# Kernel tuning notes

Hardware: AMD Instinct MI355X
Metric: run time of the kernel (lower is better)

The kernel has to match this reference:

```python
import jax, jax.numpy as jnp
from jax import lax
import numpy as np

T, B, I = 512, 64, 1024
L, H = 2, 1024

def setup_inputs() -> dict:
    key = jax.random.key(0)
    k1, k2, k3 = jax.random.split(key, 3)
    scale = 1.0 / np.sqrt(H)
    return {
        "x": jax.random.normal(k1, (T, B, I), dtype=jnp.float32),
        "w_ih": jax.random.normal(k2, (L, 4 * H, I), dtype=jnp.float32) * scale,
        "w_hh": jax.random.normal(k3, (L, 4 * H, H), dtype=jnp.float32) * scale,
        "b_ih": jnp.zeros((L, 4 * H), dtype=jnp.float32),
        "b_hh": jnp.zeros((L, 4 * H), dtype=jnp.float32),
    }

def _lstm_layer(seq, wi, wh, b):
    # seq: [T, B, D]; wi: [4H, D]; wh: [4H, H]; b: [4H]
    Bsz = seq.shape[1]
    Hh = wh.shape[1]
    # precompute input projection for all timesteps (one big GEMM)
    xin = jnp.einsum('tbd,gd->tbg', seq, wi) + b  # [T, B, 4H]
    def step(carry, xt):
        h, c = carry
        gates = xt + h @ wh.T  # [B, 4H]
        i, f, g, o = jnp.split(gates, 4, axis=1)
        c = jax.nn.sigmoid(f) * c + jax.nn.sigmoid(i) * jnp.tanh(g)
        h = jax.nn.sigmoid(o) * jnp.tanh(c)
        return (h, c), h
    h0 = jnp.zeros((Bsz, Hh), seq.dtype)
    c0 = jnp.zeros((Bsz, Hh), seq.dtype)
    (hn, cn), out = lax.scan(step, (h0, c0), xin)
    return out, hn, cn

def reference(x, w_ih, w_hh, b_ih, b_hh):
    seq = x
    h_n, c_n = [], []
    for l in range(w_hh.shape[0]):
        seq, hn, cn = _lstm_layer(seq, w_ih[l], w_hh[l], b_ih[l] + b_hh[l])
        h_n.append(hn)
        c_n.append(cn)
    return seq, jnp.stack(h_n, 0), jnp.stack(c_n, 0)
```

## Files before the change

### kernel.cpp

```cpp
#include <hip/hip_runtime.h>
#include <cstddef>
#include <cstdint>

#define T_LEN   512
#define BATCH   64
#define IN_DIM  1024
#define HID     1024
#define GATES   4096
#define NLAYERS 2
#define BH      (BATCH * HID)
#define LBLK    256
#define NBLK    512

typedef __bf16 bf16;
typedef __bf16 bf16x8 __attribute__((ext_vector_type(8)));
typedef float  f32x4  __attribute__((ext_vector_type(4)));

__global__ __launch_bounds__(256) void cvt_bf16(const float* __restrict__ in,
                                                bf16* __restrict__ out, int n4) {
    int i = blockIdx.x * blockDim.x + threadIdx.x;
    if (i >= n4) return;
    float4 v = ((const float4*)in)[i];
    bf16 o[4] = {(bf16)v.x, (bf16)v.y, (bf16)v.z, (bf16)v.w};
    *(uint2*)(out + 4 * (size_t)i) = *(uint2*)o;
}

#define GEMV8(XP, BB)                                                          \
    _Pragma("unroll")                                                          \
    for (int q = 0; q < 8; ++q) {                                              \
        const int k0 = q * 32;                                                 \
        acc0 = __builtin_amdgcn_mfma_f32_16x16x32_bf16(                        \
            *(const bf16x8*)((XP) + k0),       *(const bf16x8*)((BB) + k0),       acc0, 0, 0, 0); \
        acc1 = __builtin_amdgcn_mfma_f32_16x16x32_bf16(                        \
            *(const bf16x8*)((XP) + 256 + k0), *(const bf16x8*)((BB) + 256 + k0), acc1, 0, 0, 0); \
        acc2 = __builtin_amdgcn_mfma_f32_16x16x32_bf16(                        \
            *(const bf16x8*)((XP) + 512 + k0), *(const bf16x8*)((BB) + 512 + k0), acc2, 0, 0, 0); \
        acc3 = __builtin_amdgcn_mfma_f32_16x16x32_bf16(                        \
            *(const bf16x8*)((XP) + 768 + k0), *(const bf16x8*)((BB) + 768 + k0), acc3, 0, 0, 0); \
    }

__global__ __launch_bounds__(256) void lstm_pipe(
    const bf16*  __restrict__ wi0,
    const bf16*  __restrict__ wh0,
    const bf16*  __restrict__ wi1,
    const bf16*  __restrict__ wh1,
    const float* __restrict__ bih,
    const float* __restrict__ bhh,
    const bf16*  __restrict__ xbf,
    bf16*        __restrict__ h0seq,
    bf16*        __restrict__ h1seq,
    float*       __restrict__ outf,
    float*       __restrict__ hf0,
    float*       __restrict__ hf1,
    float*       __restrict__ cb0,
    float*       __restrict__ cb1,
    unsigned*    __restrict__ bar)
{
    __shared__ bf16  Bi[16 * 1032];
    __shared__ bf16  Bh[16 * 1032];
    __shared__ float sg[4 * 272];

    const int bk   = blockIdx.x;
    const bool isL1 = (bk >= LBLK);
    const int lk   = bk & (LBLK - 1);
    const int j0   = lk * 4;
    const int tid  = threadIdx.x;
    const int lane = tid & 63;
    const int wv   = tid >> 6;
    const int m0   = wv * 16;
    const int quad = lane >> 4;
    const int l16  = lane & 15;

    unsigned* flags   = bar;
    unsigned* release = bar + 768;

    const bf16* wiL = isL1 ? wi1 : wi0;
    const bf16* whL = isL1 ? wh1 : wh0;
    const int   boff = isL1 ? GATES : 0;
    bf16*       hW  = isL1 ? h1seq : h0seq;
    float*      hfL = isL1 ? hf1 : hf0;
    float*      cbL = isL1 ? cb1 : cb0;

    #pragma unroll
    for (int i = 0; i < 8; ++i) {
        int flat = i * 256 + tid;
        int row  = flat >> 7;
        int k16  = flat & 127;
        int grr  = (row >> 2) * 1024 + j0 + (row & 3);
        *(uint4*)&Bi[row * 1032 + k16 * 8] =
            *(const uint4*)(wiL + (size_t)grr * IN_DIM + k16 * 8);
        *(uint4*)&Bh[row * 1032 + k16 * 8] =
            *(const uint4*)(whL + (size_t)grr * HID + k16 * 8);
    }

    const int cb = m0 + l16;
    const int cu = j0 + quad;
    float c = 0.f;

    const int gr = (l16 >> 2) * 1024 + j0 + (l16 & 3);
    const float bias = bih[boff + gr] + bhh[boff + gr];

    __syncthreads();

    const bf16*  bibase = &Bi[l16 * 1032 + quad * 8];
    const bf16*  bhbase = &Bh[l16 * 1032 + quad * 8];
    const size_t arow   = (size_t)(m0 + l16) * HID + quad * 8;

    f32x4 acc0, acc1, acc2, acc3;
    if (!isL1) {
        const bf16* xp = xbf + arow;
        acc0 = {bias, bias, bias, bias};
        acc1 = {0.f, 0.f, 0.f, 0.f};
        acc2 = {0.f, 0.f, 0.f, 0.f};
        acc3 = {0.f, 0.f, 0.f, 0.f};
        GEMV8(xp, bibase)
    }

    for (int s = 0; s < T_LEN + 1; ++s) {
        if (s > 0) {
            const unsigned ep = (unsigned)s;
            if (tid == 0) {
                unsigned guard = 0;
                while (__hip_atomic_load(release, __ATOMIC_RELAXED,
                                         __HIP_MEMORY_SCOPE_AGENT) < ep) {
                    __builtin_amdgcn_s_sleep(1);
                    if (++guard > (1u << 16)) break;
                }
            }
            __syncthreads();
        }

        const bool active = isL1 ? (s >= 1) : (s < T_LEN);
        if (active) {
            const int t = isL1 ? (s - 1) : s;
            if (isL1) {
                const bf16* xp = h0seq + (size_t)t * BH + arow;
                acc0 = {bias, bias, bias, bias};
                acc1 = {0.f, 0.f, 0.f, 0.f};
                acc2 = {0.f, 0.f, 0.f, 0.f};
                acc3 = {0.f, 0.f, 0.f, 0.f};
                GEMV8(xp, bibase)
                if (t > 0) {
                    const bf16* hp = h1seq + (size_t)(t - 1) * BH + arow;
                    GEMV8(hp, bhbase)
                }
            } else {
                if (t > 0) {
                    const bf16* hp = h0seq + (size_t)(t - 1) * BH + arow;
                    GEMV8(hp, bhbase)
                }
            }

            f32x4 g4 = (acc0 + acc1) + (acc2 + acc3);

            #pragma unroll
            for (int r = 0; r < 4; ++r)
                sg[wv * 272 + (quad * 4 + r) * 17 + l16] = g4[r];
            const float* gp = &sg[wv * 272 + l16 * 17];
            float gi = gp[quad], gf = gp[4 + quad], gg = gp[8 + quad], go = gp[12 + quad];

            float si  = 1.f / (1.f + expf(-gi));
            float sf_ = 1.f / (1.f + expf(-gf));
            float so  = 1.f / (1.f + expf(-go));
            float cv  = sf_ * c + si * tanhf(gg);
            float hv  = so * tanhf(cv);
            c = cv;

            const size_t idx = (size_t)cb * HID + cu;
            float hvn = __shfl_xor(hv, 16);
            if ((quad & 1) == 0) {
                bf16 hb  = (bf16)hv;
                bf16 hbn = (bf16)hvn;
                unsigned pk = (unsigned)__builtin_bit_cast(unsigned short, hb) |
                              ((unsigned)__builtin_bit_cast(unsigned short, hbn) << 16);
                __hip_atomic_store((unsigned*)(hW + (size_t)t * BH + idx), pk,
                                   __ATOMIC_RELAXED, __HIP_MEMORY_SCOPE_AGENT);
            }
            if (isL1) outf[(size_t)t * BH + idx] = hv;
            if (t == T_LEN - 1) hfL[idx] = hv;
        }

        if (s < T_LEN) {
            const unsigned ep = (unsigned)(s + 1);
            asm volatile("s_waitcnt vmcnt(0)" ::: "memory");
            __syncthreads();
            if (tid == 0)
                __hip_atomic_store(flags + bk, ep,
                                   __ATOMIC_RELAXED, __HIP_MEMORY_SCOPE_AGENT);

            if (!isL1 && s < T_LEN - 1) {
                const bf16* xp = xbf + (size_t)(s + 1) * BH + arow;
                acc0 = {bias, bias, bias, bias};
                acc1 = {0.f, 0.f, 0.f, 0.f};
                acc2 = {0.f, 0.f, 0.f, 0.f};
                acc3 = {0.f, 0.f, 0.f, 0.f};
                GEMV8(xp, bibase)
            }

            if (bk == NBLK - 1 && tid < 64) {
                unsigned guard = 0;
                for (;;) {
                    bool good = true;
                    #pragma unroll
                    for (int j = 0; j < 8; ++j) {
                        unsigned f = __hip_atomic_load(flags + tid + 64 * j,
                                       __ATOMIC_RELAXED, __HIP_MEMORY_SCOPE_AGENT);
                        good = good && (f >= ep);
                    }
                    if (__all(good)) break;
                    __builtin_amdgcn_s_sleep(1);
                    if (++guard > (1u << 16)) break;
                }
                if (tid == 0)
                    __hip_atomic_store(release, ep,
                                       __ATOMIC_RELAXED, __HIP_MEMORY_SCOPE_AGENT);
            }
        }
    }

    cbL[(size_t)cb * HID + cu] = c;
}

extern "C" void kernel_launch(void* const* d_in, const int* in_sizes, int n_in,
                              void* d_out, int out_size, void* d_ws, size_t ws_size,
                              hipStream_t stream) {
    const float* x    = (const float*)d_in[0];
    const float* w_ih = (const float*)d_in[1];
    const float* w_hh = (const float*)d_in[2];
    const float* b_ih = (const float*)d_in[3];
    const float* b_hh = (const float*)d_in[4];
    float* out = (float*)d_out;

    const size_t seqE = (size_t)T_LEN * BATCH * HID;
    const size_t BHs  = (size_t)BATCH * HID;

    bf16* xbf   = (bf16*)d_ws;
    bf16* h0seq = xbf + seqE;
    bf16* h1seq = h0seq + seqE;
    bf16* wi0b  = h1seq + seqE;
    bf16* wh0b  = wi0b + (size_t)GATES * IN_DIM;
    bf16* wi1b  = wh0b + (size_t)GATES * HID;
    bf16* wh1b  = wi1b + (size_t)GATES * HID;
    float* hf0  = (float*)(wh1b + (size_t)GATES * HID);
    float* hf1  = hf0 + BHs;
    float* cb0  = hf1 + BHs;
    float* cb1  = cb0 + BHs;
    unsigned* bar = (unsigned*)(cb1 + BHs);

    cvt_bf16<<<(int)(seqE / 4 + 255) / 256, 256, 0, stream>>>(x, xbf, (int)(seqE / 4));
    cvt_bf16<<<(GATES * IN_DIM / 4 + 255) / 256, 256, 0, stream>>>(
        w_ih, wi0b, GATES * IN_DIM / 4);
    cvt_bf16<<<(GATES * HID / 4 + 255) / 256, 256, 0, stream>>>(
        w_hh, wh0b, GATES * HID / 4);
    cvt_bf16<<<(GATES * HID / 4 + 255) / 256, 256, 0, stream>>>(
        w_ih + (size_t)GATES * IN_DIM, wi1b, GATES * HID / 4);
    cvt_bf16<<<(GATES * HID / 4 + 255) / 256, 256, 0, stream>>>(
        w_hh + (size_t)GATES * HID, wh1b, GATES * HID / 4);

    hipMemsetAsync(bar, 0, 1024 * sizeof(unsigned), stream);

    void* args[15] = { (void*)&wi0b, (void*)&wh0b, (void*)&wi1b, (void*)&wh1b,
                       (void*)&b_ih, (void*)&b_hh, (void*)&xbf,
                       (void*)&h0seq, (void*)&h1seq, (void*)&out,
                       (void*)&hf0, (void*)&hf1, (void*)&cb0, (void*)&cb1,
                       (void*)&bar };
    hipLaunchCooperativeKernel((void*)lstm_pipe, dim3(NBLK), dim3(256),
                               args, 0, stream);

    hipMemcpyAsync(out + seqE,           hf0, BHs * sizeof(float),
                   hipMemcpyDeviceToDevice, stream);
    hipMemcpyAsync(out + seqE + BHs,     hf1, BHs * sizeof(float),
                   hipMemcpyDeviceToDevice, stream);
    hipMemcpyAsync(out + seqE + 2 * BHs, cb0, BHs * sizeof(float),
                   hipMemcpyDeviceToDevice, stream);
    hipMemcpyAsync(out + seqE + 3 * BHs, cb1, BHs * sizeof(float),
                   hipMemcpyDeviceToDevice, stream);
}
```

Baseline: 9.228 ms.

## Fuse both LSTM layers into each block and replace central barrier with distributed flag polling

Each of 256 blocks now holds the weight slices for both layers (four LDS tiles) and runs layer 0 at step s and layer 1 at step s-2 in the same iteration, so one grid sync per step covers both layers. The single releaser block that gathered all flags and published a release counter is removed. Instead every block's first wave polls all 256 flags directly. This removes a serial hop through the central block, at the cost of doubling per-block work and LDS use, putting more polling traffic on the flag array, and lowering the spin guard.

```diff
diff --git a/kernel.cpp b/kernel.cpp
--- a/kernel.cpp
+++ b/kernel.cpp
@@ -9,8 +9,7 @@
 #define GATES   4096
 #define NLAYERS 2
 #define BH      (BATCH * HID)
-#define LBLK    256
-#define NBLK    512
+#define RBLK    256
 
 typedef __bf16 bf16;
 typedef __bf16 bf16x8 __attribute__((ext_vector_type(8)));
@@ -25,21 +24,20 @@
     *(uint2*)(out + 4 * (size_t)i) = *(uint2*)o;
 }
 
-#define GEMV8(XP, BB)                                                          \
-    _Pragma("unroll")                                                          \
-    for (int q = 0; q < 8; ++q) {                                              \
-        const int k0 = q * 32;                                                 \
-        acc0 = __builtin_amdgcn_mfma_f32_16x16x32_bf16(                        \
-            *(const bf16x8*)((XP) + k0),       *(const bf16x8*)((BB) + k0),       acc0, 0, 0, 0); \
-        acc1 = __builtin_amdgcn_mfma_f32_16x16x32_bf16(                        \
-            *(const bf16x8*)((XP) + 256 + k0), *(const bf16x8*)((BB) + 256 + k0), acc1, 0, 0, 0); \
-        acc2 = __builtin_amdgcn_mfma_f32_16x16x32_bf16(                        \
-            *(const bf16x8*)((XP) + 512 + k0), *(const bf16x8*)((BB) + 512 + k0), acc2, 0, 0, 0); \
-        acc3 = __builtin_amdgcn_mfma_f32_16x16x32_bf16(                        \
-            *(const bf16x8*)((XP) + 768 + k0), *(const bf16x8*)((BB) + 768 + k0), acc3, 0, 0, 0); \
+__device__ __forceinline__ void gemv8(f32x4 acc[4], const bf16* __restrict__ xp,
+                                      const bf16* __restrict__ bb) {
+    #pragma unroll
+    for (int q = 0; q < 8; ++q) {
+        const int k0 = q * 32;
+        #pragma unroll
+        for (int ch = 0; ch < 4; ++ch)
+            acc[ch] = __builtin_amdgcn_mfma_f32_16x16x32_bf16(
+                *(const bf16x8*)(xp + ch * 256 + k0),
+                *(const bf16x8*)(bb + ch * 256 + k0), acc[ch], 0, 0, 0);
     }
-
-__global__ __launch_bounds__(256) void lstm_pipe(
+}
+
+__global__ __launch_bounds__(256) void lstm_fused(
     const bf16*  __restrict__ wi0,
     const bf16*  __restrict__ wh0,
     const bf16*  __restrict__ wi1,
@@ -54,16 +52,16 @@
     float*       __restrict__ hf1,
     float*       __restrict__ cb0,
     float*       __restrict__ cb1,
-    unsigned*    __restrict__ bar)
+    unsigned*    __restrict__ flags)
 {
-    __shared__ bf16  Bi[16 * 1032];
-    __shared__ bf16  Bh[16 * 1032];
+    __shared__ bf16  B0i[16 * 1032];
+    __shared__ bf16  B0h[16 * 1032];
+    __shared__ bf16  B1i[16 * 1032];
+    __shared__ bf16  B1h[16 * 1032];
     __shared__ float sg[4 * 272];
 
     const int bk   = blockIdx.x;
-    const bool isL1 = (bk >= LBLK);
-    const int lk   = bk & (LBLK - 1);
-    const int j0   = lk * 4;
+    const int j0   = bk * 4;
     const int tid  = threadIdx.x;
     const int lane = tid & 63;
     const int wv   = tid >> 6;
@@ -71,154 +69,147 @@
     const int quad = lane >> 4;
     const int l16  = lane & 15;
 
-    unsigned* flags   = bar;
-    unsigned* release = bar + 768;
-
-    const bf16* wiL = isL1 ? wi1 : wi0;
-    const bf16* whL = isL1 ? wh1 : wh0;
-    const int   boff = isL1 ? GATES : 0;
-    bf16*       hW  = isL1 ? h1seq : h0seq;
-    float*      hfL = isL1 ? hf1 : hf0;
-    float*      cbL = isL1 ? cb1 : cb0;
-
     #pragma unroll
     for (int i = 0; i < 8; ++i) {
         int flat = i * 256 + tid;
         int row  = flat >> 7;
         int k16  = flat & 127;
         int grr  = (row >> 2) * 1024 + j0 + (row & 3);
-        *(uint4*)&Bi[row * 1032 + k16 * 8] =
-            *(const uint4*)(wiL + (size_t)grr * IN_DIM + k16 * 8);
-        *(uint4*)&Bh[row * 1032 + k16 * 8] =
-            *(const uint4*)(whL + (size_t)grr * HID + k16 * 8);
+        *(uint4*)&B0i[row * 1032 + k16 * 8] =
+            *(const uint4*)(wi0 + (size_t)grr * IN_DIM + k16 * 8);
+        *(uint4*)&B0h[row * 1032 + k16 * 8] =
+            *(const uint4*)(wh0 + (size_t)grr * HID + k16 * 8);
+        *(uint4*)&B1i[row * 1032 + k16 * 8] =
+            *(const uint4*)(wi1 + (size_t)grr * HID + k16 * 8);
+        *(uint4*)&B1h[row * 1032 + k16 * 8] =
+            *(const uint4*)(wh1 + (size_t)grr * HID + k16 * 8);
     }
 
     const int cb = m0 + l16;
     const int cu = j0 + quad;
-    float c = 0.f;
+    float c0 = 0.f, c1 = 0.f;
 
     const int gr = (l16 >> 2) * 1024 + j0 + (l16 & 3);
-    const float bias = bih[boff + gr] + bhh[boff + gr];
+    const float bias0 = bih[gr] + bhh[gr];
+    const float bias1 = bih[GATES + gr] + bhh[GATES + gr];
 
     __syncthreads();
 
-    const bf16*  bibase = &Bi[l16 * 1032 + quad * 8];
-    const bf16*  bhbase = &Bh[l16 * 1032 + quad * 8];
-    const size_t arow   = (size_t)(m0 + l16) * HID + quad * 8;
-
-    f32x4 acc0, acc1, acc2, acc3;
-    if (!isL1) {
-        const bf16* xp = xbf + arow;
-        acc0 = {bias, bias, bias, bias};
-        acc1 = {0.f, 0.f, 0.f, 0.f};
-        acc2 = {0.f, 0.f, 0.f, 0.f};
-        acc3 = {0.f, 0.f, 0.f, 0.f};
-        GEMV8(xp, bibase)
-    }
-
-    for (int s = 0; s < T_LEN + 1; ++s) {
+    const bf16*  b0i = &B0i[l16 * 1032 + quad * 8];
+    const bf16*  b0h = &B0h[l16 * 1032 + quad * 8];
+    const bf16*  b1i = &B1i[l16 * 1032 + quad * 8];
+    const bf16*  b1h = &B1h[l16 * 1032 + quad * 8];
+    const size_t arow = (size_t)(m0 + l16) * HID + quad * 8;
+    const size_t idx  = (size_t)cb * HID + cu;
+
+    f32x4 p0[4], p1[4] = {};
+    p0[0] = {bias0, bias0, bias0, bias0};
+    p0[1] = {0.f, 0.f, 0.f, 0.f};
+    p0[2] = {0.f, 0.f, 0.f, 0.f};
+    p0[3] = {0.f, 0.f, 0.f, 0.f};
+    gemv8(p0, xbf + arow, b0i);
+
+    for (int s = 0; s <= T_LEN + 1; ++s) {
         if (s > 0) {
             const unsigned ep = (unsigned)s;
-            if (tid == 0) {
+            if (wv == 0) {
                 unsigned guard = 0;
-                while (__hip_atomic_load(release, __ATOMIC_RELAXED,
-                                         __HIP_MEMORY_SCOPE_AGENT) < ep) {
+                for (;;) {
+                    bool good = true;
+                    #pragma unroll
+                    for (int j = 0; j < 4; ++j) {
+                        unsigned f = __hip_atomic_load(flags + lane + 64 * j,
+                                       __ATOMIC_RELAXED, __HIP_MEMORY_SCOPE_AGENT);
+                        good = good && (f >= ep);
+                    }
+                    if (__all(good)) break;
                     __builtin_amdgcn_s_sleep(1);
-                    if (++guard > (1u << 16)) break;
+                    if (++guard > (1u << 13)) break;
                 }
             }
             __syncthreads();
         }
 
-        const bool active = isL1 ? (s >= 1) : (s < T_LEN);
-        if (active) {
-            const int t = isL1 ? (s - 1) : s;
-            if (isL1) {
-                const bf16* xp = h0seq + (size_t)t * BH + arow;
-                acc0 = {bias, bias, bias, bias};
-                acc1 = {0.f, 0.f, 0.f, 0.f};
-                acc2 = {0.f, 0.f, 0.f, 0.f};
-                acc3 = {0.f, 0.f, 0.f, 0.f};
-                GEMV8(xp, bibase)
-                if (t > 0) {
-                    const bf16* hp = h1seq + (size_t)(t - 1) * BH + arow;
-                    GEMV8(hp, bhbase)
-                }
-            } else {
-                if (t > 0) {
-                    const bf16* hp = h0seq + (size_t)(t - 1) * BH + arow;
-                    GEMV8(hp, bhbase)
-                }
-            }
-
-            f32x4 g4 = (acc0 + acc1) + (acc2 + acc3);
-
+        if (s < T_LEN) {
+            if (s > 0) gemv8(p0, h0seq + (size_t)(s - 1) * BH + arow, b0h);
+            f32x4 g4 = (p0[0] + p0[1]) + (p0[2] + p0[3]);
             #pragma unroll
             for (int r = 0; r < 4; ++r)
                 sg[wv * 272 + (quad * 4 + r) * 17 + l16] = g4[r];
             const float* gp = &sg[wv * 272 + l16 * 17];
             float gi = gp[quad], gf = gp[4 + quad], gg = gp[8 + quad], go = gp[12 + quad];
-
             float si  = 1.f / (1.f + expf(-gi));
             float sf_ = 1.f / (1.f + expf(-gf));
             float so  = 1.f / (1.f + expf(-go));
-            float cv  = sf_ * c + si * tanhf(gg);
+            float cv  = sf_ * c0 + si * tanhf(gg);
             float hv  = so * tanhf(cv);
-            c = cv;
-
-            const size_t idx = (size_t)cb * HID + cu;
+            c0 = cv;
             float hvn = __shfl_xor(hv, 16);
             if ((quad & 1) == 0) {
                 bf16 hb  = (bf16)hv;
                 bf16 hbn = (bf16)hvn;
                 unsigned pk = (unsigned)__builtin_bit_cast(unsigned short, hb) |
                               ((unsigned)__builtin_bit_cast(unsigned short, hbn) << 16);
-                __hip_atomic_store((unsigned*)(hW + (size_t)t * BH + idx), pk,
+                __hip_atomic_store((unsigned*)(h0seq + (size_t)s * BH + idx), pk,
                                    __ATOMIC_RELAXED, __HIP_MEMORY_SCOPE_AGENT);
             }
-            if (isL1) outf[(size_t)t * BH + idx] = hv;
-            if (t == T_LEN - 1) hfL[idx] = hv;
-        }
-
-        if (s < T_LEN) {
-            const unsigned ep = (unsigned)(s + 1);
+            if (s == T_LEN - 1) hf0[idx] = hv;
+        }
+
+        if (s >= 2) {
+            const int t = s - 2;
+            if (t > 0) gemv8(p1, h1seq + (size_t)(t - 1) * BH + arow, b1h);
+            f32x4 g4 = (p1[0] + p1[1]) + (p1[2] + p1[3]);
+            #pragma unroll
+            for (int r = 0; r < 4; ++r)
+                sg[wv * 272 + (quad * 4 + r) * 17 + l16] = g4[r];
+            const float* gp = &sg[wv * 272 + l16 * 17];
+            float gi = gp[quad], gf = gp[4 + quad], gg = gp[8 + quad], go = gp[12 + quad];
+            float si  = 1.f / (1.f + expf(-gi));
+            float sf_ = 1.f / (1.f + expf(-gf));
+            float so  = 1.f / (1.f + expf(-go));
+            float cv  = sf_ * c1 + si * tanhf(gg);
+            float hv  = so * tanhf(cv);
+            c1 = cv;
+            float hvn = __shfl_xor(hv, 16);
+            if ((quad & 1) == 0) {
+                bf16 hb  = (bf16)hv;
+                bf16 hbn = (bf16)hvn;
+                unsigned pk = (unsigned)__builtin_bit_cast(unsigned short, hb) |
+                              ((unsigned)__builtin_bit_cast(unsigned short, hbn) << 16);
+                __hip_atomic_store((unsigned*)(h1seq + (size_t)t * BH + idx), pk,
+                                   __ATOMIC_RELAXED, __HIP_MEMORY_SCOPE_AGENT);
+            }
+            outf[(size_t)t * BH + idx] = hv;
+            if (t == T_LEN - 1) hf1[idx] = hv;
+        }
+
+        if (s <= T_LEN) {
             asm volatile("s_waitcnt vmcnt(0)" ::: "memory");
             __syncthreads();
             if (tid == 0)
-                __hip_atomic_store(flags + bk, ep,
+                __hip_atomic_store(flags + bk, (unsigned)(s + 1),
                                    __ATOMIC_RELAXED, __HIP_MEMORY_SCOPE_AGENT);
 
-            if (!isL1 && s < T_LEN - 1) {
-                const bf16* xp = xbf + (size_t)(s + 1) * BH + arow;
-                acc0 = {bias, bias, bias, bias};
-                acc1 = {0.f, 0.f, 0.f, 0.f};
-                acc2 = {0.f, 0.f, 0.f, 0.f};
-                acc3 = {0.f, 0.f, 0.f, 0.f};
-                GEMV8(xp, bibase)
-            }
-
-            if (bk == NBLK - 1 && tid < 64) {
-                unsigned guard = 0;
-                for (;;) {
-                    bool good = true;
-                    #pragma unroll
-                    for (int j = 0; j < 8; ++j) {
-                        unsigned f = __hip_atomic_load(flags + tid + 64 * j,
-                                       __ATOMIC_RELAXED, __HIP_MEMORY_SCOPE_AGENT);
-                        good = good && (f >= ep);
-                    }
-                    if (__all(good)) break;
-                    __builtin_amdgcn_s_sleep(1);
-                    if (++guard > (1u << 16)) break;
-                }
-                if (tid == 0)
-                    __hip_atomic_store(release, ep,
-                                       __ATOMIC_RELAXED, __HIP_MEMORY_SCOPE_AGENT);
+            if (s < T_LEN - 1) {
+                p0[0] = {bias0, bias0, bias0, bias0};
+                p0[1] = {0.f, 0.f, 0.f, 0.f};
+                p0[2] = {0.f, 0.f, 0.f, 0.f};
+                p0[3] = {0.f, 0.f, 0.f, 0.f};
+                gemv8(p0, xbf + (size_t)(s + 1) * BH + arow, b0i);
+            }
+            if (s >= 1) {
+                p1[0] = {bias1, bias1, bias1, bias1};
+                p1[1] = {0.f, 0.f, 0.f, 0.f};
+                p1[2] = {0.f, 0.f, 0.f, 0.f};
+                p1[3] = {0.f, 0.f, 0.f, 0.f};
+                gemv8(p1, h0seq + (size_t)(s - 1) * BH + arow, b1i);
             }
         }
     }
 
-    cbL[(size_t)cb * HID + cu] = c;
+    cb0[idx] = c0;
+    cb1[idx] = c1;
 }
 
 extern "C" void kernel_launch(void* const* d_in, const int* in_sizes, int n_in,
@@ -245,7 +236,7 @@
     float* hf1  = hf0 + BHs;
     float* cb0  = hf1 + BHs;
     float* cb1  = cb0 + BHs;
-    unsigned* bar = (unsigned*)(cb1 + BHs);
+    unsigned* flags = (unsigned*)(cb1 + BHs);
 
     cvt_bf16<<<(int)(seqE / 4 + 255) / 256, 256, 0, stream>>>(x, xbf, (int)(seqE / 4));
     cvt_bf16<<<(GATES * IN_DIM / 4 + 255) / 256, 256, 0, stream>>>(
@@ -257,14 +248,14 @@
     cvt_bf16<<<(GATES * HID / 4 + 255) / 256, 256, 0, stream>>>(
         w_hh + (size_t)GATES * HID, wh1b, GATES * HID / 4);
 
-    hipMemsetAsync(bar, 0, 1024 * sizeof(unsigned), stream);
+    hipMemsetAsync(flags, 0, 512 * sizeof(unsigned), stream);
 
     void* args[15] = { (void*)&wi0b, (void*)&wh0b, (void*)&wi1b, (void*)&wh1b,
                        (void*)&b_ih, (void*)&b_hh, (void*)&xbf,
                        (void*)&h0seq, (void*)&h1seq, (void*)&out,
                        (void*)&hf0, (void*)&hf1, (void*)&cb0, (void*)&cb1,
-                       (void*)&bar };
-    hipLaunchCooperativeKernel((void*)lstm_pipe, dim3(NBLK), dim3(256),
+                       (void*)&flags };
+    hipLaunchCooperativeKernel((void*)lstm_fused, dim3(RBLK), dim3(256),
                                args, 0, stream);
 
     hipMemcpyAsync(out + seqE,           hf0, BHs * sizeof(float),
```

Result: faster. 8.704 ms (-5.7%).
